# Performance work log

Hardware: AMD Instinct MI355X
Metric: run time of the kernel (lower is better)

## Reference

```python
import jax, jax.numpy as jnp
import numpy as np

B, L, D, H = 1, 320, 128, 4
DH = D // H
LN_EPS = 1e-5


def setup_inputs() -> dict:
    key = jax.random.key(0)
    ks = jax.random.split(key, 4)
    z = jax.random.normal(ks[0], (B, L, L, D), jnp.float32)
    mask = jax.random.randint(ks[1], (B, L), 0, 2).astype(jnp.int32)
    ln_g = jnp.ones((D,), jnp.float32)
    ln_b = jnp.zeros((D,), jnp.float32)
    w_qkv = (jax.random.normal(ks[2], (3 * D, D), jnp.float32) * 0.02)
    b_qkv = jnp.zeros((3 * D,), jnp.float32)
    w_out = (jax.random.normal(ks[3], (D, D), jnp.float32) * 0.02)
    b_out = jnp.zeros((D,), jnp.float32)
    return {"z": z, "mask": mask, "ln_g": ln_g, "ln_b": ln_b,
            "w_qkv": w_qkv, "b_qkv": b_qkv, "w_out": w_out, "b_out": b_out}


def reference(z, mask, ln_g, ln_b, w_qkv, b_qkv, w_out, b_out):
    # z: (B, L, L, D), mask: (B, L) with 1 = keep, 0 = masked key
    mu = jnp.mean(z, axis=-1, keepdims=True)
    var = jnp.mean(jnp.square(z - mu), axis=-1, keepdims=True)
    zn = (z - mu) * jax.lax.rsqrt(var + LN_EPS) * ln_g + ln_b

    zf = zn.reshape(B * L, L, D)                       # row-wise: each of B*L rows is a length-L sequence
    qkv = zf @ w_qkv.T + b_qkv                         # (B*L, L, 3D)
    q, k, v = jnp.split(qkv, 3, axis=-1)

    def split_heads(x):
        return x.reshape(B * L, L, H, DH).transpose(0, 2, 1, 3)  # (B*L, H, L, DH)

    q, k, v = split_heads(q), split_heads(k), split_heads(v)
    scores = jnp.einsum('nhqd,nhkd->nhqk', q, k) / np.sqrt(DH).astype(np.float32)

    # additive -inf at masked key positions, shared across all L rows of a batch
    bias = jnp.where(mask > 0, 0.0, -jnp.inf).astype(scores.dtype)   # (B, L)
    bias = jnp.repeat(bias, L, axis=0)[:, None, None, :]             # (B*L, 1, 1, L)

    attn = jax.nn.softmax(scores + bias, axis=-1)
    o = jnp.einsum('nhqk,nhkd->nhqd', attn, v)
    o = o.transpose(0, 2, 1, 3).reshape(B * L, L, D)
    out = o @ w_out.T + b_out
    return z + out.reshape(B, L, L, D)
```

## Files before the change

### kernel.cpp

```cpp
#include <hip/hip_runtime.h>

#define LQ 320
#define NSEQ 320
#define NROWS (NSEQ*LQ)
#define DDIM 128
#define NH 4
#define DHD 32
#define LN_EPS 1e-5f
#define QSC2 0.25508652025545527f

typedef __bf16 bf16x8 __attribute__((ext_vector_type(8)));
typedef float f32x4 __attribute__((ext_vector_type(4)));
union FragU { unsigned int u[4]; bf16x8 v; };

__device__ int g_inv[LQ];
__device__ int g_cnt;
__device__ __align__(16) unsigned short g_wbf[512 * DDIM];

__device__ inline unsigned short f2bf(float f) {
    unsigned int u = __float_as_uint(f);
    u += 0x7fffu + ((u >> 16) & 1u);
    return (unsigned short)(u >> 16);
}
__device__ inline unsigned int pack2(float a, float b) {
    return (unsigned int)f2bf(a) | ((unsigned int)f2bf(b) << 16);
}

__global__ __launch_bounds__(256) void k0_ln(
    const float* __restrict__ z, const float* __restrict__ ln_g, const float* __restrict__ ln_b,
    unsigned int* __restrict__ znws, const int* __restrict__ mask,
    const float* __restrict__ w_qkv, const float* __restrict__ w_out)
{
    const int tid = threadIdx.x;
    const int bx = blockIdx.x;
    const int rowbase = bx * 64;
    const int lane = tid & 63;
    const int wid = tid >> 6;

    if (bx == 0) {
        if (tid < 64) {
            int carry = 0;
            #pragma unroll 1
            for (int c = 0; c < 5; ++c) {
                const int i = c * 64 + tid;
                const int m = (mask[i] > 0) ? 1 : 0;
                int v = m;
                #pragma unroll
                for (int off = 1; off < 64; off <<= 1) {
                    const int o = __shfl_up(v, off, 64);
                    if (tid >= off) v += o;
                }
                v += carry;
                if (m) g_inv[v - 1] = i;
                carry = __shfl(v, 63, 64);
            }
            if (tid == 0) g_cnt = carry;
            for (int s = carry + tid; s < LQ; s += 64) g_inv[s] = 0;
        }
    } else if (bx <= 64) {
        const int idx = (bx - 1) * 256 + tid;
        const float4 w4 = (idx < 12288) ? ((const float4*)w_qkv)[idx]
                                        : ((const float4*)w_out)[idx - 12288];
        uint2 val;
        val.x = pack2(w4.x, w4.y);
        val.y = pack2(w4.z, w4.w);
        ((uint2*)g_wbf)[idx] = val;
    }

    const float g0 = ln_g[2 * lane], g1 = ln_g[2 * lane + 1];
    const float bb0 = ln_b[2 * lane], bb1 = ln_b[2 * lane + 1];
    #pragma unroll 1
    for (int r = wid; r < 64; r += 4) {
        const int row = rowbase + r;
        const float2 v = *(const float2*)(z + (size_t)row * DDIM + 2 * lane);
        float s = v.x + v.y;
        float s2 = v.x * v.x + v.y * v.y;
        #pragma unroll
        for (int off = 32; off > 0; off >>= 1) {
            s  += __shfl_xor(s, off, 64);
            s2 += __shfl_xor(s2, off, 64);
        }
        const float mu = s * (1.0f / 128.0f);
        const float var = s2 * (1.0f / 128.0f) - mu * mu;
        const float rs = rsqrtf(var + LN_EPS);
        znws[(size_t)row * 64 + lane] =
            pack2((v.x - mu) * rs * g0 + bb0, (v.y - mu) * rs * g1 + bb1);
    }
}

__global__ __launch_bounds__(256, 4) void k1_qkv(
    const unsigned short* __restrict__ znws, const float* __restrict__ b_qkv,
    unsigned short* __restrict__ qws, unsigned short* __restrict__ kws,
    unsigned short* __restrict__ vws)
{
    __shared__ unsigned short tr[8704];
    const int tid = threadIdx.x;
    const int bx = blockIdx.x;
    const int sect = bx % 3;
    const int mbase = (bx / 3) * 128;
    const int lane = tid & 63;
    const int wid = tid >> 6;
    const int qn = lane & 15, gd = lane >> 4;

    const int cnt = __builtin_amdgcn_readfirstlane(g_cnt);
    const int PT16 = (cnt + 15) & ~15;
    const int CP8  = (cnt + 7) & ~7;
    const int stride = (sect == 0) ? LQ : ((sect == 1) ? PT16 : CP8);
    const int rows_total = NSEQ * stride;
    if (mbase >= rows_total) return;

    const int n0 = mbase / stride;
    const int s0 = mbase - n0 * stride;

    int arow[2];
    #pragma unroll
    for (int rg = 0; rg < 2; ++rg) {
        const int off = wid * 32 + rg * 16 + qn;
        int n = n0, s = s0 + off;
        while (s >= stride) { s -= stride; ++n; }
        int grow = n * LQ + ((sect == 0) ? s : g_inv[s]);
        if (mbase + off >= rows_total) grow = 0;
        arow[rg] = grow;
    }

    const f32x4 zero4 = {0.f, 0.f, 0.f, 0.f};
    f32x4 acc[2][8];
    #pragma unroll
    for (int rg = 0; rg < 2; ++rg)
        #pragma unroll
        for (int nt = 0; nt < 8; ++nt) acc[rg][nt] = zero4;

    #pragma unroll
    for (int kt = 0; kt < 4; ++kt) {
        FragU af[2];
        #pragma unroll
        for (int rg = 0; rg < 2; ++rg)
            af[rg].v = *(const bf16x8*)&znws[(size_t)arow[rg] * DDIM + kt * 32 + gd * 8];
        #pragma unroll
        for (int nt = 0; nt < 8; ++nt) {
            FragU bf;
            bf.v = *(const bf16x8*)&g_wbf[(size_t)(sect * 128 + nt * 16 + qn) * DDIM + kt * 32 + gd * 8];
            #pragma unroll
            for (int rg = 0; rg < 2; ++rg)
                acc[rg][nt] = __builtin_amdgcn_mfma_f32_16x16x32_bf16(af[rg].v, bf.v, acc[rg][nt], 0, 0, 0);
        }
    }

    float bq[8];
    #pragma unroll
    for (int nt = 0; nt < 8; ++nt) bq[nt] = b_qkv[sect * 128 + nt * 16 + qn];
    const float sc = (sect == 0) ? QSC2 : 1.0f;

    #pragma unroll 1
    for (int p = 0; p < 2; ++p) {
        if ((wid >> 1) == p) {
            const int wl = wid & 1;
            #pragma unroll
            for (int rg = 0; rg < 2; ++rg) {
                #pragma unroll
                for (int r = 0; r < 4; ++r) {
                    const int lr = wl * 32 + rg * 16 + 4 * gd + r;
                    #pragma unroll
                    for (int nt = 0; nt < 8; ++nt) {
                        const int col = nt * 16 + qn;
                        const unsigned short val = f2bf((acc[rg][nt][r] + bq[nt]) * sc);
                        if (sect < 2) tr[lr * 132 + col] = val;
                        else          tr[col * 68 + lr] = val;
                    }
                }
            }
        }
        __syncthreads();

        if (sect < 2) {
            unsigned short* dst = (sect == 0) ? qws : kws;
            #pragma unroll 1
            for (int k8 = 0; k8 < 8; ++k8) {
                const int o2 = lane * 4 + k8 * 256;
                const int i_loc = o2 >> 5, d = o2 & 31;
                const int off = p * 64 + i_loc;
                if (mbase + off < rows_total) {
                    int n = n0, s = s0 + off;
                    while (s >= stride) { s -= stride; ++n; }
                    const ushort4 val = *(const ushort4*)&tr[i_loc * 132 + wid * 32 + d];
                    *(ushort4*)&dst[((size_t)(n * NH + wid) * LQ + s) * DHD + d] = val;
                }
            }
        } else {
            #pragma unroll 1
            for (int k8 = 0; k8 < 8; ++k8) {
                const int o2 = lane * 4 + k8 * 256;
                const int d = o2 >> 6, i_loc = o2 & 63;
                const int off = p * 64 + i_loc;
                if (mbase + off < rows_total) {
                    int n = n0, s = s0 + off;
                    while (s >= stride) { s -= stride; ++n; }
                    const ushort4 val = *(const ushort4*)&tr[(wid * 32 + d) * 68 + i_loc];
                    *(ushort4*)&vws[(size_t)(n * NH + wid) * (DHD * LQ) + d * CP8 + s] = val;
                }
            }
        }
        if (p == 0) __syncthreads();
    }
}

#define KSTR 20
__global__ __launch_bounds__(256, 4) void k2_attn_mfma(
    const unsigned short* __restrict__ qws, const unsigned short* __restrict__ kws,
    const unsigned short* __restrict__ vtws, unsigned short* __restrict__ ows)
{
    __shared__ unsigned int kT[LQ * KSTR];
    const int tid = threadIdx.x;
    const int bx = blockIdx.x;
    const int nh = bx / 5;
    const int qs = bx - nh * 5;
    const int lane = tid & 63;
    const int wid = tid >> 6;
    const int qn = lane & 15;
    const int gd = lane >> 4;

    const int cnt = __builtin_amdgcn_readfirstlane(g_cnt);
    const int PT  = (cnt + 15) & ~15;
    const int CP8 = (cnt + 7) & ~7;
    const int NCH = (PT + 159) / 160;

    const uint4* kp4 = (const uint4*)(kws + (size_t)nh * LQ * DHD);
    #pragma unroll 1
    for (int idx = tid; idx < PT * 4; idx += 256) {
        const int r = idx >> 2, c4 = idx & 3;
        *(uint4*)&kT[r * KSTR + 4 * c4] = kp4[idx];
    }
    __syncthreads();

    const f32x4 zero4 = {0.f, 0.f, 0.f, 0.f};
    const int alo = (((gd & 1) << 5) | qn) << 2;
    const int ahi = alo + 64;
    const bool hiT = (gd >= 2);
    const int n = nh >> 2, h = nh & 3;
    const unsigned short* vbase = vtws + (size_t)nh * DHD * LQ;

    const int qt = qs * 4 + wid;

    FragU qf;
    qf.v = *(const bf16x8*)(qws + ((size_t)nh * LQ + qt * 16 + qn) * DHD + 8 * gd);

    f32x4 o0 = zero4, o1 = zero4;
    float m_run = -1e30f;
    float l_run = 0.f;

    #pragma unroll 1
    for (int ch = 0; ch < NCH; ++ch) {
        const int tb = ch * 10;

        f32x4 st[10];
        #pragma unroll
        for (int kt = 0; kt < 10; ++kt) {
            const int ktg = tb + kt;
            if (ktg * 16 < cnt) {
                FragU kf;
                const uint4 kv = *(const uint4*)&kT[(ktg * 16 + qn) * KSTR + 4 * gd];
                kf.u[0] = kv.x; kf.u[1] = kv.y; kf.u[2] = kv.z; kf.u[3] = kv.w;
                f32x4 c0 = zero4;
                if ((ktg + 1) * 16 > cnt) {
                    const int jb = ktg * 16 + 4 * gd;
                    #pragma unroll
                    for (int r = 0; r < 4; ++r)
                        c0[r] = (jb + r < cnt) ? 0.f : -1e30f;
                }
                st[kt] = __builtin_amdgcn_mfma_f32_16x16x32_bf16(kf.v, qf.v, c0, 0, 0, 0);
            }
        }

        float mh = -1e30f;
        #pragma unroll
        for (int kt = 0; kt < 10; ++kt)
            if ((tb + kt) * 16 < cnt)
                mh = fmaxf(mh, fmaxf(fmaxf(st[kt][0], st[kt][1]), fmaxf(st[kt][2], st[kt][3])));
        mh = fmaxf(mh, __shfl_xor(mh, 16, 64));
        mh = fmaxf(mh, __shfl_xor(mh, 32, 64));
        const float m_new = fmaxf(m_run, mh);
        const float scl = __builtin_amdgcn_exp2f(m_run - m_new);
        m_run = m_new;
        l_run *= scl;
        o0 *= scl;
        o1 *= scl;

        #pragma unroll
        for (int kt = 0; kt < 10; ++kt) {
            if ((tb + kt) * 16 < cnt) {
                st[kt][0] = __builtin_amdgcn_exp2f(st[kt][0] - m_new);
                st[kt][1] = __builtin_amdgcn_exp2f(st[kt][1] - m_new);
                st[kt][2] = __builtin_amdgcn_exp2f(st[kt][2] - m_new);
                st[kt][3] = __builtin_amdgcn_exp2f(st[kt][3] - m_new);
                l_run += st[kt][0] + st[kt][1] + st[kt][2] + st[kt][3];
            } else {
                st[kt] = zero4;
            }
        }

        #pragma unroll
        for (int kc = 0; kc < 5; ++kc) {
            if ((tb + 2 * kc) * 16 < cnt) {
                const int t0 = 2 * kc, t1 = 2 * kc + 1;
                const unsigned int p01a = pack2(st[t0][0], st[t0][1]);
                const unsigned int p23a = pack2(st[t0][2], st[t0][3]);
                const unsigned int p01b = pack2(st[t1][0], st[t1][1]);
                const unsigned int p23b = pack2(st[t1][2], st[t1][3]);
                FragU pa;
                {
                    const int a0 = __builtin_amdgcn_ds_bpermute(alo, (int)p01a);
                    const int b0 = __builtin_amdgcn_ds_bpermute(alo, (int)p01b);
                    const int a1 = __builtin_amdgcn_ds_bpermute(alo, (int)p23a);
                    const int b1 = __builtin_amdgcn_ds_bpermute(alo, (int)p23b);
                    const int a2 = __builtin_amdgcn_ds_bpermute(ahi, (int)p01a);
                    const int b2 = __builtin_amdgcn_ds_bpermute(ahi, (int)p01b);
                    const int a3 = __builtin_amdgcn_ds_bpermute(ahi, (int)p23a);
                    const int b3 = __builtin_amdgcn_ds_bpermute(ahi, (int)p23b);
                    pa.u[0] = (unsigned int)(hiT ? b0 : a0);
                    pa.u[1] = (unsigned int)(hiT ? b1 : a1);
                    pa.u[2] = (unsigned int)(hiT ? b2 : a2);
                    pa.u[3] = (unsigned int)(hiT ? b3 : a3);
                }
                FragU bv0, bv1;
                const int koff = ch * 160 + 32 * kc + 8 * gd;
                bv0.v = *(const bf16x8*)(vbase + (size_t)qn * CP8 + koff);
                bv1.v = *(const bf16x8*)(vbase + (size_t)(16 + qn) * CP8 + koff);
                o0 = __builtin_amdgcn_mfma_f32_16x16x32_bf16(pa.v, bv0.v, o0, 0, 0, 0);
                o1 = __builtin_amdgcn_mfma_f32_16x16x32_bf16(pa.v, bv1.v, o1, 0, 0, 0);
            }
        }
    }

    l_run += __shfl_xor(l_run, 16, 64);
    l_run += __shfl_xor(l_run, 32, 64);
    const float inv = 1.0f / l_run;

    #pragma unroll
    for (int r = 0; r < 4; ++r) {
        const int qg = qt * 16 + 4 * gd + r;
        unsigned short* orow = ows + ((size_t)(n * LQ + qg)) * DDIM + h * DHD + qn;
        orow[0]  = f2bf(o0[r] * inv);
        orow[16] = f2bf(o1[r] * inv);
    }
}

__global__ __launch_bounds__(256, 4) void k3_out(
    const unsigned short* __restrict__ ows,
    const float* __restrict__ b_out, const float* __restrict__ z,
    float* __restrict__ out)
{
    const int tid = threadIdx.x;
    const int mbase = blockIdx.x * 128;
    const int lane = tid & 63;
    const int wid = tid >> 6;
    const int qn = lane & 15, gd = lane >> 4;

    const f32x4 zero4 = {0.f, 0.f, 0.f, 0.f};
    f32x4 acc[2][8];
    #pragma unroll
    for (int rg = 0; rg < 2; ++rg)
        #pragma unroll
        for (int nt = 0; nt < 8; ++nt) acc[rg][nt] = zero4;

    #pragma unroll
    for (int kt = 0; kt < 4; ++kt) {
        FragU af[2];
        #pragma unroll
        for (int rg = 0; rg < 2; ++rg)
            af[rg].v = *(const bf16x8*)&ows[
                (size_t)(mbase + wid * 32 + rg * 16 + qn) * DDIM + kt * 32 + gd * 8];
        #pragma unroll
        for (int nt = 0; nt < 8; ++nt) {
            FragU bf;
            bf.v = *(const bf16x8*)&g_wbf[(size_t)(384 + nt * 16 + qn) * DDIM + kt * 32 + gd * 8];
            #pragma unroll
            for (int rg = 0; rg < 2; ++rg)
                acc[rg][nt] = __builtin_amdgcn_mfma_f32_16x16x32_bf16(af[rg].v, bf.v, acc[rg][nt], 0, 0, 0);
        }
    }

    float bb[8];
    #pragma unroll
    for (int nt = 0; nt < 8; ++nt) bb[nt] = b_out[nt * 16 + qn];

    #pragma unroll
    for (int rg = 0; rg < 2; ++rg) {
        #pragma unroll
        for (int r = 0; r < 4; ++r) {
            const int grow = mbase + wid * 32 + rg * 16 + 4 * gd + r;
            const float* zr = z + (size_t)grow * DDIM;
            float* outr = out + (size_t)grow * DDIM;
            #pragma unroll
            for (int nt = 0; nt < 8; ++nt) {
                const int cg = nt * 16 + qn;
                outr[cg] = acc[rg][nt][r] + bb[nt] + zr[cg];
            }
        }
    }
}

extern "C" void kernel_launch(void* const* d_in, const int* in_sizes, int n_in,
                              void* d_out, int out_size, void* d_ws, size_t ws_size,
                              hipStream_t stream) {
    const float* z     = (const float*)d_in[0];
    const int*   mask  = (const int*)d_in[1];
    const float* ln_g  = (const float*)d_in[2];
    const float* ln_b  = (const float*)d_in[3];
    const float* w_qkv = (const float*)d_in[4];
    const float* b_qkv = (const float*)d_in[5];
    const float* w_out = (const float*)d_in[6];
    const float* b_out = (const float*)d_in[7];
    float* out = (float*)d_out;

    unsigned short* ws = (unsigned short*)d_ws;
    const size_t qE = (size_t)NSEQ * NH * LQ * DHD;
    unsigned short* qws = ws;
    unsigned short* kws = qws + qE;
    unsigned short* vws = kws + qE;
    unsigned short* shared_rgn = vws + qE;
    unsigned int*   znws = (unsigned int*)shared_rgn;
    unsigned short* ows  = shared_rgn;

    hipLaunchKernelGGL(k0_ln, dim3(NROWS / 64), dim3(256), 0, stream,
                       z, ln_g, ln_b, znws, mask, w_qkv, w_out);
    hipLaunchKernelGGL(k1_qkv, dim3(2400), dim3(256), 0, stream,
                       (const unsigned short*)znws, b_qkv, qws, kws, vws);
    hipLaunchKernelGGL(k2_attn_mfma, dim3(6400), dim3(256), 0, stream,
                       qws, kws, vws, ows);
    hipLaunchKernelGGL(k3_out, dim3(800), dim3(256), 0, stream,
                       ows, b_out, z, out);
}
```

Measured before the change: 242.7 us.

## Pre-swizzle bf16 weights into MFMA fragment order and stage them in LDS

The weight conversion now writes bf16 weights in per-lane MFMA fragment order, so each 16-byte chunk maps directly to one lane's B operand. The QKV and output-projection kernels copy their 32KB weight slice into LDS with coalesced uint4 loads and read B fragments from LDS instead of strided global loads. The QKV epilogue transpose buffer now reuses that larger LDS region, which lets all four waves write their tiles at once and drops the two-pass write/sync loop. The cost is 32-34KB of LDS per block, which may lower occupancy, plus an extra weight copy and barrier at the start of every block.

```diff
diff --git a/kernel.cpp b/kernel.cpp
--- a/kernel.cpp
+++ b/kernel.cpp
@@ -57,14 +57,25 @@
             if (tid == 0) g_cnt = carry;
             for (int s = carry + tid; s < LQ; s += 64) g_inv[s] = 0;
         }
-    } else if (bx <= 64) {
-        const int idx = (bx - 1) * 256 + tid;
-        const float4 w4 = (idx < 12288) ? ((const float4*)w_qkv)[idx]
-                                        : ((const float4*)w_out)[idx - 12288];
-        uint2 val;
-        val.x = pack2(w4.x, w4.y);
-        val.y = pack2(w4.z, w4.w);
-        ((uint2*)g_wbf)[idx] = val;
+    } else if (bx <= 32) {
+        const int cid = (bx - 1) * 256 + tid;
+        const int l2  = cid & 63;
+        const int nt  = (cid >> 6) & 7;
+        const int kt  = (cid >> 9) & 3;
+        const int s4  = cid >> 11;
+        const int qn2 = l2 & 15, gd2 = l2 >> 4;
+        const int row = s4 * 128 + nt * 16 + qn2;
+        const float4* src4 = (s4 < 3) ? (const float4*)w_qkv : (const float4*)w_out;
+        const int rloc = (s4 < 3) ? row : (row - 384);
+        const int fi = rloc * 32 + kt * 8 + gd2 * 2;
+        const float4 a = src4[fi];
+        const float4 b = src4[fi + 1];
+        uint4 val;
+        val.x = pack2(a.x, a.y);
+        val.y = pack2(a.z, a.w);
+        val.z = pack2(b.x, b.y);
+        val.w = pack2(b.z, b.w);
+        ((uint4*)g_wbf)[cid] = val;
     }
 
     const float g0 = ln_g[2 * lane], g1 = ln_g[2 * lane + 1];
@@ -93,7 +104,7 @@
     unsigned short* __restrict__ qws, unsigned short* __restrict__ kws,
     unsigned short* __restrict__ vws)
 {
-    __shared__ unsigned short tr[8704];
+    __shared__ unsigned short ldsb[17408];
     const int tid = threadIdx.x;
     const int bx = blockIdx.x;
     const int sect = bx % 3;
@@ -109,6 +120,13 @@
     const int rows_total = NSEQ * stride;
     if (mbase >= rows_total) return;
 
+    {
+        const uint4* src = (const uint4*)g_wbf + sect * 2048;
+        uint4* dst = (uint4*)ldsb;
+        #pragma unroll
+        for (int i = 0; i < 8; ++i) dst[tid + i * 256] = src[tid + i * 256];
+    }
+
     const int n0 = mbase / stride;
     const int s0 = mbase - n0 * stride;
 
@@ -123,6 +141,8 @@
         arow[rg] = grow;
     }
 
+    __syncthreads();
+
     const f32x4 zero4 = {0.f, 0.f, 0.f, 0.f};
     f32x4 acc[2][8];
     #pragma unroll
@@ -139,7 +159,7 @@
         #pragma unroll
         for (int nt = 0; nt < 8; ++nt) {
             FragU bf;
-            bf.v = *(const bf16x8*)&g_wbf[(size_t)(sect * 128 + nt * 16 + qn) * DDIM + kt * 32 + gd * 8];
+            bf.v = *(const bf16x8*)&ldsb[((kt * 8 + nt) * 64 + lane) * 8];
             #pragma unroll
             for (int rg = 0; rg < 2; ++rg)
                 acc[rg][nt] = __builtin_amdgcn_mfma_f32_16x16x32_bf16(af[rg].v, bf.v, acc[rg][nt], 0, 0, 0);
@@ -151,56 +171,50 @@
     for (int nt = 0; nt < 8; ++nt) bq[nt] = b_qkv[sect * 128 + nt * 16 + qn];
     const float sc = (sect == 0) ? QSC2 : 1.0f;
 
-    #pragma unroll 1
-    for (int p = 0; p < 2; ++p) {
-        if ((wid >> 1) == p) {
-            const int wl = wid & 1;
+    __syncthreads();
+    unsigned short* tr = ldsb;
+
+    #pragma unroll
+    for (int rg = 0; rg < 2; ++rg) {
+        #pragma unroll
+        for (int r = 0; r < 4; ++r) {
+            const int row = wid * 32 + rg * 16 + 4 * gd + r;
             #pragma unroll
-            for (int rg = 0; rg < 2; ++rg) {
-                #pragma unroll
-                for (int r = 0; r < 4; ++r) {
-                    const int lr = wl * 32 + rg * 16 + 4 * gd + r;
-                    #pragma unroll
-                    for (int nt = 0; nt < 8; ++nt) {
-                        const int col = nt * 16 + qn;
-                        const unsigned short val = f2bf((acc[rg][nt][r] + bq[nt]) * sc);
-                        if (sect < 2) tr[lr * 132 + col] = val;
-                        else          tr[col * 68 + lr] = val;
-                    }
-                }
-            }
-        }
-        __syncthreads();
-
-        if (sect < 2) {
-            unsigned short* dst = (sect == 0) ? qws : kws;
-            #pragma unroll 1
-            for (int k8 = 0; k8 < 8; ++k8) {
-                const int o2 = lane * 4 + k8 * 256;
-                const int i_loc = o2 >> 5, d = o2 & 31;
-                const int off = p * 64 + i_loc;
-                if (mbase + off < rows_total) {
-                    int n = n0, s = s0 + off;
-                    while (s >= stride) { s -= stride; ++n; }
-                    const ushort4 val = *(const ushort4*)&tr[i_loc * 132 + wid * 32 + d];
-                    *(ushort4*)&dst[((size_t)(n * NH + wid) * LQ + s) * DHD + d] = val;
-                }
-            }
-        } else {
-            #pragma unroll 1
-            for (int k8 = 0; k8 < 8; ++k8) {
-                const int o2 = lane * 4 + k8 * 256;
-                const int d = o2 >> 6, i_loc = o2 & 63;
-                const int off = p * 64 + i_loc;
-                if (mbase + off < rows_total) {
-                    int n = n0, s = s0 + off;
-                    while (s >= stride) { s -= stride; ++n; }
-                    const ushort4 val = *(const ushort4*)&tr[(wid * 32 + d) * 68 + i_loc];
-                    *(ushort4*)&vws[(size_t)(n * NH + wid) * (DHD * LQ) + d * CP8 + s] = val;
-                }
-            }
-        }
-        if (p == 0) __syncthreads();
+            for (int nt = 0; nt < 8; ++nt) {
+                const int col = nt * 16 + qn;
+                const unsigned short val = f2bf((acc[rg][nt][r] + bq[nt]) * sc);
+                if (sect < 2) tr[row * 132 + col] = val;
+                else          tr[col * 132 + row] = val;
+            }
+        }
+    }
+    __syncthreads();
+
+    if (sect < 2) {
+        unsigned short* dst = (sect == 0) ? qws : kws;
+        #pragma unroll 1
+        for (int k16 = 0; k16 < 16; ++k16) {
+            const int o2 = lane * 4 + k16 * 256;
+            const int i_loc = o2 >> 5, d = o2 & 31;
+            if (mbase + i_loc < rows_total) {
+                int n = n0, s = s0 + i_loc;
+                while (s >= stride) { s -= stride; ++n; }
+                const ushort4 val = *(const ushort4*)&tr[i_loc * 132 + wid * 32 + d];
+                *(ushort4*)&dst[((size_t)(n * NH + wid) * LQ + s) * DHD + d] = val;
+            }
+        }
+    } else {
+        #pragma unroll 1
+        for (int k16 = 0; k16 < 16; ++k16) {
+            const int o2 = lane * 4 + k16 * 256;
+            const int d = o2 >> 7, i_loc = o2 & 127;
+            if (mbase + i_loc < rows_total) {
+                int n = n0, s = s0 + i_loc;
+                while (s >= stride) { s -= stride; ++n; }
+                const ushort4 val = *(const ushort4*)&tr[(wid * 32 + d) * 132 + i_loc];
+                *(ushort4*)&vws[(size_t)(n * NH + wid) * (DHD * LQ) + d * CP8 + s] = val;
+            }
+        }
     }
 }
 
@@ -349,12 +363,21 @@
     const float* __restrict__ b_out, const float* __restrict__ z,
     float* __restrict__ out)
 {
+    __shared__ unsigned short ldsb[16384];
     const int tid = threadIdx.x;
     const int mbase = blockIdx.x * 128;
     const int lane = tid & 63;
     const int wid = tid >> 6;
     const int qn = lane & 15, gd = lane >> 4;
 
+    {
+        const uint4* src = (const uint4*)g_wbf + 3 * 2048;
+        uint4* dst = (uint4*)ldsb;
+        #pragma unroll
+        for (int i = 0; i < 8; ++i) dst[tid + i * 256] = src[tid + i * 256];
+    }
+    __syncthreads();
+
     const f32x4 zero4 = {0.f, 0.f, 0.f, 0.f};
     f32x4 acc[2][8];
     #pragma unroll
@@ -372,7 +395,7 @@
         #pragma unroll
         for (int nt = 0; nt < 8; ++nt) {
             FragU bf;
-            bf.v = *(const bf16x8*)&g_wbf[(size_t)(384 + nt * 16 + qn) * DDIM + kt * 32 + gd * 8];
+            bf.v = *(const bf16x8*)&ldsb[((kt * 8 + nt) * 64 + lane) * 8];
             #pragma unroll
             for (int rg = 0; rg < 2; ++rg)
                 acc[rg][nt] = __builtin_amdgcn_mfma_f32_16x16x32_bf16(af[rg].v, bf.v, acc[rg][nt], 0, 0, 0);
```

New measurement: 211.3 us. 1.15x faster.
